# Performance work log

Hardware: AMD Instinct MI355X
Metric: run time of the kernel (lower is better)

The kernel has to match this reference:

```python
import jax, jax.numpy as jnp
import numpy as np

N_NODES = 50000


def gcn_conv(x, edge_index, W, b):
    """PyG-style GCNConv: add self-loops, symmetric normalization, x@W + bias."""
    N = x.shape[0]
    loop = jnp.arange(N, dtype=edge_index.dtype)
    src = jnp.concatenate([edge_index[0], loop])  # message sources
    dst = jnp.concatenate([edge_index[1], loop])  # aggregation targets
    deg = jax.ops.segment_sum(jnp.ones_like(dst, dtype=x.dtype), dst, num_segments=N)
    dinv = jnp.where(deg > 0, jax.lax.rsqrt(jnp.maximum(deg, 1.0)), 0.0)
    norm = dinv[src] * dinv[dst]  # [E+N]
    h = x @ W  # [N, out] dense transform first (fewer edge-dim FLOPs)
    msg = h[src] * norm[:, None]  # [E+N, out] gathered, normalized messages
    out = jax.ops.segment_sum(msg, dst, num_segments=N)
    return out + b


def setup_inputs() -> dict:
    key = jax.random.key(0)
    k1, k2, k3, k4 = jax.random.split(key, 4)
    x = jax.random.normal(k1, (N_NODES, 256), dtype=jnp.float32)
    edge_index = jax.random.randint(k2, (2, 800000), 0, N_NODES, dtype=jnp.int64)
    W1 = jax.random.normal(k3, (256, 256), dtype=jnp.float32) * (1.0 / np.sqrt(256))
    b1 = jnp.zeros((256,), dtype=jnp.float32)
    W2 = jax.random.normal(k4, (256, 128), dtype=jnp.float32) * (1.0 / np.sqrt(256))
    b2 = jnp.zeros((128,), dtype=jnp.float32)
    return {"x": x, "edge_index": edge_index, "W1": W1, "b1": b1, "W2": W2, "b2": b2}


def reference(x, edge_index, W1, b1, W2, b2):
    h = gcn_conv(x, edge_index, W1, b1)
    h = jax.nn.relu(h)
    return gcn_conv(h, edge_index, W2, b2)
```

## Files before the change

kernel.cpp:

```cpp
#include <hip/hip_runtime.h>

#define N_FEAT_IN 256
#define N_HID 256
#define N_OUT 128

using f32x4 = __attribute__((ext_vector_type(4))) float;
using bf16x8 = __attribute__((ext_vector_type(8))) short;

__device__ inline unsigned short bf16_rne(float f) {
    unsigned u = __builtin_bit_cast(unsigned, f);
    unsigned r = u + 0x7FFFu + ((u >> 16) & 1u);
    return (unsigned short)(r >> 16);
}
__device__ inline float bf16_to_f(unsigned short h) {
    unsigned u = ((unsigned)h) << 16;
    return __builtin_bit_cast(float, u);
}

__global__ void detect_i64_kernel(const int* __restrict__ edges, int* __restrict__ flag) {
    __shared__ int s[256];
    int tid = threadIdx.x;
    int zeros = 0;
    for (int i = tid; i < 2048; i += 256) zeros += (edges[2 * i + 1] == 0) ? 1 : 0;
    s[tid] = zeros;
    __syncthreads();
    for (int off = 128; off; off >>= 1) {
        if (tid < off) s[tid] += s[tid + off];
        __syncthreads();
    }
    if (tid == 0) flag[0] = (s[0] > 1900) ? 1 : 0;
}

__global__ void convert_count_kernel(const void* __restrict__ edges, int E,
                                     const int* __restrict__ flag,
                                     int* __restrict__ src, int* __restrict__ dst,
                                     int* __restrict__ cnt) {
    int e = blockIdx.x * blockDim.x + threadIdx.x;
    if (e >= E) return;
    int s, d;
    if (flag[0]) {
        const long long* p = (const long long*)edges;
        s = (int)p[e];
        d = (int)p[(size_t)E + e];
    } else {
        const int* p = (const int*)edges;
        s = p[e];
        d = p[(size_t)E + e];
    }
    src[e] = s;
    dst[e] = d;
    atomicAdd(&cnt[d], 1);
}

__global__ __launch_bounds__(256) void scan_block_kernel(
    const int* __restrict__ cnt, int Nn, int* __restrict__ rowp, int* __restrict__ bsum,
    float* __restrict__ dinv) {
    __shared__ int sd[256];
    const int tid = threadIdx.x;
    const int i = blockIdx.x * 256 + tid;
    const int v = (i < Nn) ? cnt[i] : 0;
    if (i < Nn) dinv[i] = rsqrtf((float)(v + 1));
    sd[tid] = v;
    __syncthreads();
    for (int off = 1; off < 256; off <<= 1) {
        int t = (tid >= off) ? sd[tid - off] : 0;
        __syncthreads();
        sd[tid] += t;
        __syncthreads();
    }
    if (i < Nn) rowp[i] = sd[tid] - v;
    if (tid == 255) bsum[blockIdx.x] = sd[255];
}

__global__ __launch_bounds__(256) void scan_top_kernel(
    int* __restrict__ bsum, int Nb, int* __restrict__ rowp, int Nn) {
    __shared__ int sd[256];
    const int tid = threadIdx.x;
    const int v = (tid < Nb) ? bsum[tid] : 0;
    sd[tid] = v;
    __syncthreads();
    for (int off = 1; off < 256; off <<= 1) {
        int t = (tid >= off) ? sd[tid - off] : 0;
        __syncthreads();
        sd[tid] += t;
        __syncthreads();
    }
    if (tid < Nb) bsum[tid] = sd[tid] - v;
    if (tid == 255) rowp[Nn] = sd[255];
}

__global__ __launch_bounds__(256) void scan_add_kernel(
    const int* __restrict__ bsum, int Nn, int* __restrict__ rowp, int* __restrict__ cursor) {
    const int i = blockIdx.x * 256 + threadIdx.x;
    if (i < Nn) {
        const int r = rowp[i] + bsum[i >> 8];
        rowp[i] = r;
        cursor[i] = r;
    }
}

__global__ void fill_kernel(const int* __restrict__ src, const int* __restrict__ dst, int E,
                            const float* __restrict__ dinv, int* __restrict__ cursor,
                            int2* __restrict__ ce) {
    int e = blockIdx.x * blockDim.x + threadIdx.x;
    if (e >= E) return;
    int s = src[e], d = dst[e];
    int pos = atomicAdd(&cursor[d], 1);
    float w = dinv[s] * dinv[d];
    ce[pos] = make_int2(s, __builtin_bit_cast(int, w));
}

__global__ __launch_bounds__(256) void split_kernel(
    const float* __restrict__ in, int n4,
    unsigned short* __restrict__ hi, unsigned short* __restrict__ lo) {
    int i = blockIdx.x * 256 + threadIdx.x;
    if (i >= n4) return;
    float4 v = ((const float4*)in)[i];
    ushort4 h, l;
    h.x = bf16_rne(v.x); l.x = bf16_rne(v.x - bf16_to_f(h.x));
    h.y = bf16_rne(v.y); l.y = bf16_rne(v.y - bf16_to_f(h.y));
    h.z = bf16_rne(v.z); l.z = bf16_rne(v.z - bf16_to_f(h.z));
    h.w = bf16_rne(v.w); l.w = bf16_rne(v.w - bf16_to_f(h.w));
    ((ushort4*)hi)[i] = h;
    ((ushort4*)lo)[i] = l;
}

__global__ __launch_bounds__(256) void splitT_kernel(
    const float* __restrict__ W, int K, int N,
    unsigned short* __restrict__ thi, unsigned short* __restrict__ tlo) {
    int idx = blockIdx.x * 256 + threadIdx.x;
    if (idx >= K * N) return;
    int k = idx / N, n = idx - k * N;
    float f = W[idx];
    unsigned short h = bf16_rne(f);
    unsigned short l = bf16_rne(f - bf16_to_f(h));
    thi[(size_t)n * K + k] = h;
    tlo[(size_t)n * K + k] = l;
}

__global__ __launch_bounds__(256) void gemm_mfma_kernel(
    const unsigned short* __restrict__ Ah, const unsigned short* __restrict__ Al,
    const unsigned short* __restrict__ Bh, const unsigned short* __restrict__ Bl,
    unsigned short* __restrict__ C, int M, int N, int K) {
    __shared__ char lds[4 * 128 * 64];
    char* As_h = lds;
    char* As_l = lds + 8192;
    char* Bs_h = lds + 16384;
    char* Bs_l = lds + 24576;

    const int tid = threadIdx.x;
    const int lane = tid & 63;
    const int wv = tid >> 6;
    const int wrow = (wv >> 1) * 64;
    const int wcol = (wv & 1) * 64;

    const int srow = tid >> 1;
    const int shalf = tid & 1;

    const long arow_g = (long)blockIdx.y * 128 + srow;
    const bool aval = arow_g < M;
    const int bcol_g = blockIdx.x * 128 + srow;

    const size_t a_base = (size_t)(aval ? arow_g : 0) * K + shalf * 16;
    const size_t b_base = (size_t)bcol_g * K + shalf * 16;

    const int sw = ((srow >> 1) & 3) << 4;
    const int w0 = (srow * 64 + shalf * 32) ^ sw;
    const int w1 = (srow * 64 + shalf * 32 + 16) ^ sw;

    int ra[4], rb[4];
#pragma unroll
    for (int m = 0; m < 4; m++) {
        int r = wrow + m * 16 + (lane & 15);
        ra[m] = (r * 64 + (lane >> 4) * 16) ^ (((r >> 1) & 3) << 4);
        int c = wcol + m * 16 + (lane & 15);
        rb[m] = (c * 64 + (lane >> 4) * 16) ^ (((c >> 1) & 3) << 4);
    }

    f32x4 acc[4][4] = {};
    const bf16x8 zero8 = {0, 0, 0, 0, 0, 0, 0, 0};

    const int nkt = K >> 5;
    for (int kt = 0; kt < nkt; kt++) {
        const int kb = kt * 32;
        bf16x8 vah0 = zero8, vah1 = zero8, val0 = zero8, val1 = zero8;
        if (aval) {
            vah0 = *(const bf16x8*)(Ah + a_base + kb);
            vah1 = *(const bf16x8*)(Ah + a_base + kb + 8);
            val0 = *(const bf16x8*)(Al + a_base + kb);
            val1 = *(const bf16x8*)(Al + a_base + kb + 8);
        }
        bf16x8 vbh0 = *(const bf16x8*)(Bh + b_base + kb);
        bf16x8 vbh1 = *(const bf16x8*)(Bh + b_base + kb + 8);
        bf16x8 vbl0 = *(const bf16x8*)(Bl + b_base + kb);
        bf16x8 vbl1 = *(const bf16x8*)(Bl + b_base + kb + 8);
        __syncthreads();
        *(bf16x8*)(As_h + w0) = vah0;  *(bf16x8*)(As_h + w1) = vah1;
        *(bf16x8*)(As_l + w0) = val0;  *(bf16x8*)(As_l + w1) = val1;
        *(bf16x8*)(Bs_h + w0) = vbh0;  *(bf16x8*)(Bs_h + w1) = vbh1;
        *(bf16x8*)(Bs_l + w0) = vbl0;  *(bf16x8*)(Bs_l + w1) = vbl1;
        __syncthreads();
        bf16x8 ah[4], al[4], bh[4], bl[4];
#pragma unroll
        for (int m = 0; m < 4; m++) {
            ah[m] = *(const bf16x8*)(As_h + ra[m]);
            al[m] = *(const bf16x8*)(As_l + ra[m]);
            bh[m] = *(const bf16x8*)(Bs_h + rb[m]);
            bl[m] = *(const bf16x8*)(Bs_l + rb[m]);
        }
#pragma unroll
        for (int m = 0; m < 4; m++)
#pragma unroll
            for (int n = 0; n < 4; n++) {
                acc[m][n] = __builtin_amdgcn_mfma_f32_16x16x32_bf16(ah[m], bh[n], acc[m][n], 0, 0, 0);
                acc[m][n] = __builtin_amdgcn_mfma_f32_16x16x32_bf16(al[m], bh[n], acc[m][n], 0, 0, 0);
                acc[m][n] = __builtin_amdgcn_mfma_f32_16x16x32_bf16(ah[m], bl[n], acc[m][n], 0, 0, 0);
            }
    }

    const int c0 = blockIdx.x * 128 + wcol + (lane & 15);
    const long r0 = (long)blockIdx.y * 128 + wrow + (lane >> 4) * 4;
#pragma unroll
    for (int m = 0; m < 4; m++)
#pragma unroll
        for (int j = 0; j < 4; j++) {
            long r = r0 + m * 16 + j;
            if (r < M) {
#pragma unroll
                for (int n = 0; n < 4; n++)
                    C[(size_t)r * N + c0 + n * 16] = bf16_rne(acc[m][n][j]);
            }
        }
}

template <int C, bool RELU, bool SPLIT>
__global__ __launch_bounds__(256) void agg_kernel(
    const unsigned short* __restrict__ h, const int* __restrict__ rowp,
    const int2* __restrict__ ce,
    const float* __restrict__ dinv, const float* __restrict__ bias,
    float* __restrict__ out,
    unsigned short* __restrict__ ohi, unsigned short* __restrict__ olo, int Nn) {
    constexpr int VEC = C / 64;
    static_assert(VEC == 2 || VEC == 4, "C must be 128 or 256");
    const int lane = threadIdx.x & 63;
    const int wv = threadIdx.x >> 6;
    const int node0 = blockIdx.x * 4 + wv;
    if (node0 >= Nn) return;
    const int node = __builtin_amdgcn_readfirstlane(node0);
    const float di = dinv[node];
    const int coff = lane * VEC;
    const unsigned short* __restrict__ hc = h + coff;
    float acc[VEC];

    auto loadrow = [&](int row, float v[VEC]) {
        const unsigned short* r = hc + (size_t)row * C;
        if constexpr (VEC == 4) {
            ushort4 t = *(const ushort4*)r;
            v[0] = bf16_to_f(t.x); v[1] = bf16_to_f(t.y);
            v[2] = bf16_to_f(t.z); v[3] = bf16_to_f(t.w);
        } else {
            ushort2 t = *(const ushort2*)r;
            v[0] = bf16_to_f(t.x); v[1] = bf16_to_f(t.y);
        }
    };

    {
        float v[VEC];
        loadrow(node, v);
#pragma unroll
        for (int j = 0; j < VEC; j++) acc[j] = di * di * v[j];
    }

    const int s = rowp[node];
    const int e = rowp[node + 1];
    for (int base = s; base < e; base += 64) {
        const int m = min(64, e - base);
        int myc = 0, myn = 0;
        if (lane < m) {
            int2 p = ce[base + lane];
            myc = p.x;
            myn = p.y;
        }
        int j = 0;
        for (; j + 4 <= m; j += 4) {
            const int c0 = __builtin_amdgcn_readlane(myc, j);
            const int c1 = __builtin_amdgcn_readlane(myc, j + 1);
            const int c2 = __builtin_amdgcn_readlane(myc, j + 2);
            const int c3 = __builtin_amdgcn_readlane(myc, j + 3);
            const float w0 = __builtin_bit_cast(float, __builtin_amdgcn_readlane(myn, j));
            const float w1 = __builtin_bit_cast(float, __builtin_amdgcn_readlane(myn, j + 1));
            const float w2 = __builtin_bit_cast(float, __builtin_amdgcn_readlane(myn, j + 2));
            const float w3 = __builtin_bit_cast(float, __builtin_amdgcn_readlane(myn, j + 3));
            float v0[VEC], v1[VEC], v2[VEC], v3[VEC];
            loadrow(c0, v0);
            loadrow(c1, v1);
            loadrow(c2, v2);
            loadrow(c3, v3);
#pragma unroll
            for (int q = 0; q < VEC; q++)
                acc[q] += w0 * v0[q] + w1 * v1[q] + w2 * v2[q] + w3 * v3[q];
        }
        for (; j < m; ++j) {
            const int c0 = __builtin_amdgcn_readlane(myc, j);
            const float w0 = __builtin_bit_cast(float, __builtin_amdgcn_readlane(myn, j));
            float v0[VEC];
            loadrow(c0, v0);
#pragma unroll
            for (int q = 0; q < VEC; q++) acc[q] += w0 * v0[q];
        }
    }

    {
        const float* bv = bias + coff;
#pragma unroll
        for (int j = 0; j < VEC; j++) {
            acc[j] += bv[j];
            if (RELU) acc[j] = fmaxf(acc[j], 0.f);
        }
    }
    if constexpr (SPLIT) {
        if constexpr (VEC == 4) {
            ushort4 hh, ll;
            hh.x = bf16_rne(acc[0]); ll.x = bf16_rne(acc[0] - bf16_to_f(hh.x));
            hh.y = bf16_rne(acc[1]); ll.y = bf16_rne(acc[1] - bf16_to_f(hh.y));
            hh.z = bf16_rne(acc[2]); ll.z = bf16_rne(acc[2] - bf16_to_f(hh.z));
            hh.w = bf16_rne(acc[3]); ll.w = bf16_rne(acc[3] - bf16_to_f(hh.w));
            *(ushort4*)(ohi + (size_t)node * C + coff) = hh;
            *(ushort4*)(olo + (size_t)node * C + coff) = ll;
        } else {
            ushort2 hh, ll;
            hh.x = bf16_rne(acc[0]); ll.x = bf16_rne(acc[0] - bf16_to_f(hh.x));
            hh.y = bf16_rne(acc[1]); ll.y = bf16_rne(acc[1] - bf16_to_f(hh.y));
            *(ushort2*)(ohi + (size_t)node * C + coff) = hh;
            *(ushort2*)(olo + (size_t)node * C + coff) = ll;
        }
    } else {
        float* o = out + (size_t)node * C + coff;
        if constexpr (VEC == 4) {
            *(float4*)o = make_float4(acc[0], acc[1], acc[2], acc[3]);
        } else {
            *(float2*)o = make_float2(acc[0], acc[1]);
        }
    }
}

extern "C" void kernel_launch(void* const* d_in, const int* in_sizes, int n_in,
                              void* d_out, int out_size, void* d_ws, size_t ws_size,
                              hipStream_t stream) {
    const float* x = (const float*)d_in[0];
    const void* edges = d_in[1];
    const float* W1 = (const float*)d_in[2];
    const float* b1 = (const float*)d_in[3];
    const float* W2 = (const float*)d_in[4];
    const float* b2 = (const float*)d_in[5];
    float* out = (float*)d_out;

    const int Nn = in_sizes[0] / N_FEAT_IN;
    const int E = in_sizes[1] / 2;

    char* w = (char*)d_ws;
    size_t off = 0;
    auto alloc = [&](size_t bytes) -> void* {
        void* p = (void*)(w + off);
        off += (bytes + 255) & ~(size_t)255;
        return p;
    };
    int* flag = (int*)alloc(sizeof(int));
    int* srcI = (int*)alloc((size_t)E * 4);
    int* dstI = (int*)alloc((size_t)E * 4);
    int* cnt = (int*)alloc((size_t)Nn * 4);
    int* rowp = (int*)alloc(((size_t)Nn + 1) * 4);
    int* cursor = (int*)alloc((size_t)Nn * 4);
    int* bsum = (int*)alloc(1024 * 4);
    int2* ce = (int2*)alloc((size_t)E * 8);
    float* dinv = (float*)alloc((size_t)Nn * 4);
    unsigned short* xhi = (unsigned short*)alloc((size_t)Nn * N_FEAT_IN * 2);
    unsigned short* xlo = (unsigned short*)alloc((size_t)Nn * N_FEAT_IN * 2);
    unsigned short* w1hi = (unsigned short*)alloc((size_t)N_FEAT_IN * N_HID * 2);
    unsigned short* w1lo = (unsigned short*)alloc((size_t)N_FEAT_IN * N_HID * 2);
    unsigned short* w2hi = (unsigned short*)alloc((size_t)N_HID * N_OUT * 2);
    unsigned short* w2lo = (unsigned short*)alloc((size_t)N_HID * N_OUT * 2);
    unsigned short* h = (unsigned short*)alloc((size_t)Nn * N_HID * 2);
    unsigned short* a1hi = xhi;
    unsigned short* a1lo = xlo;

    hipMemsetAsync(cnt, 0, (size_t)Nn * 4, stream);
    detect_i64_kernel<<<1, 256, 0, stream>>>((const int*)edges, flag);
    const int eb = (E + 255) / 256;
    convert_count_kernel<<<eb, 256, 0, stream>>>(edges, E, flag, srcI, dstI, cnt);
    const int nb = (Nn + 255) / 256;
    scan_block_kernel<<<nb, 256, 0, stream>>>(cnt, Nn, rowp, bsum, dinv);
    scan_top_kernel<<<1, 256, 0, stream>>>(bsum, nb, rowp, Nn);
    scan_add_kernel<<<nb, 256, 0, stream>>>(bsum, Nn, rowp, cursor);
    fill_kernel<<<eb, 256, 0, stream>>>(srcI, dstI, E, dinv, cursor, ce);

    const int n4x = Nn * N_FEAT_IN / 4;
    split_kernel<<<(n4x + 255) / 256, 256, 0, stream>>>(x, n4x, xhi, xlo);
    splitT_kernel<<<(N_FEAT_IN * N_HID + 255) / 256, 256, 0, stream>>>(W1, N_FEAT_IN, N_HID, w1hi, w1lo);
    splitT_kernel<<<(N_HID * N_OUT + 255) / 256, 256, 0, stream>>>(W2, N_HID, N_OUT, w2hi, w2lo);

    dim3 g1(N_HID / 128, (Nn + 127) / 128);
    gemm_mfma_kernel<<<g1, 256, 0, stream>>>(xhi, xlo, w1hi, w1lo, h, Nn, N_HID, N_FEAT_IN);
    agg_kernel<N_HID, true, true><<<(Nn + 3) / 4, 256, 0, stream>>>(
        h, rowp, ce, dinv, b1, nullptr, a1hi, a1lo, Nn);

    dim3 g2(N_OUT / 128, (Nn + 127) / 128);
    gemm_mfma_kernel<<<g2, 256, 0, stream>>>(a1hi, a1lo, w2hi, w2lo, h, Nn, N_OUT, N_HID);
    agg_kernel<N_OUT, false, false><<<(Nn + 3) / 4, 256, 0, stream>>>(
        h, rowp, ce, dinv, b2, out, nullptr, nullptr, Nn);
}
```

Before: 261.9 us.

## Fuse x bf16 split into first GEMM and drop intermediate edge arrays

The first GEMM now reads fp32 x directly and splits it into bf16 hi/lo inside the kernel, replacing the separate split pass and its 2x bf16 intermediate buffers. The edge conversion kernel no longer writes int32 src/dst arrays; count and fill read the raw edge_index directly. This cuts a full pass over x (about 51MB read plus writes) and the edge scratch traffic. In exchange the GEMM does conversion arithmetic per tile and reads twice as many A bytes, once for each of its two column blocks.

```diff
diff --git a/kernel.cpp b/kernel.cpp
--- a/kernel.cpp
+++ b/kernel.cpp
@@ -31,24 +31,16 @@
     if (tid == 0) flag[0] = (s[0] > 1900) ? 1 : 0;
 }
 
-__global__ void convert_count_kernel(const void* __restrict__ edges, int E,
-                                     const int* __restrict__ flag,
-                                     int* __restrict__ src, int* __restrict__ dst,
-                                     int* __restrict__ cnt) {
+__global__ void count_kernel(const void* __restrict__ edges, int E,
+                             const int* __restrict__ flag, int* __restrict__ cnt) {
     int e = blockIdx.x * blockDim.x + threadIdx.x;
     if (e >= E) return;
-    int s, d;
+    int d;
     if (flag[0]) {
-        const long long* p = (const long long*)edges;
-        s = (int)p[e];
-        d = (int)p[(size_t)E + e];
+        d = (int)((const long long*)edges)[(size_t)E + e];
     } else {
-        const int* p = (const int*)edges;
-        s = p[e];
-        d = p[(size_t)E + e];
-    }
-    src[e] = s;
-    dst[e] = d;
+        d = ((const int*)edges)[(size_t)E + e];
+    }
     atomicAdd(&cnt[d], 1);
 }
 
@@ -99,30 +91,25 @@
     }
 }
 
-__global__ void fill_kernel(const int* __restrict__ src, const int* __restrict__ dst, int E,
+__global__ void fill_kernel(const void* __restrict__ edges, int E,
+                            const int* __restrict__ flag,
                             const float* __restrict__ dinv, int* __restrict__ cursor,
                             int2* __restrict__ ce) {
     int e = blockIdx.x * blockDim.x + threadIdx.x;
     if (e >= E) return;
-    int s = src[e], d = dst[e];
+    int s, d;
+    if (flag[0]) {
+        const long long* p = (const long long*)edges;
+        s = (int)p[e];
+        d = (int)p[(size_t)E + e];
+    } else {
+        const int* p = (const int*)edges;
+        s = p[e];
+        d = p[(size_t)E + e];
+    }
     int pos = atomicAdd(&cursor[d], 1);
     float w = dinv[s] * dinv[d];
     ce[pos] = make_int2(s, __builtin_bit_cast(int, w));
-}
-
-__global__ __launch_bounds__(256) void split_kernel(
-    const float* __restrict__ in, int n4,
-    unsigned short* __restrict__ hi, unsigned short* __restrict__ lo) {
-    int i = blockIdx.x * 256 + threadIdx.x;
-    if (i >= n4) return;
-    float4 v = ((const float4*)in)[i];
-    ushort4 h, l;
-    h.x = bf16_rne(v.x); l.x = bf16_rne(v.x - bf16_to_f(h.x));
-    h.y = bf16_rne(v.y); l.y = bf16_rne(v.y - bf16_to_f(h.y));
-    h.z = bf16_rne(v.z); l.z = bf16_rne(v.z - bf16_to_f(h.z));
-    h.w = bf16_rne(v.w); l.w = bf16_rne(v.w - bf16_to_f(h.w));
-    ((ushort4*)hi)[i] = h;
-    ((ushort4*)lo)[i] = l;
 }
 
 __global__ __launch_bounds__(256) void splitT_kernel(
@@ -136,6 +123,114 @@
     unsigned short l = bf16_rne(f - bf16_to_f(h));
     thi[(size_t)n * K + k] = h;
     tlo[(size_t)n * K + k] = l;
+}
+
+__global__ __launch_bounds__(256) void gemm_mfma_f32a_kernel(
+    const float* __restrict__ Af,
+    const unsigned short* __restrict__ Bh, const unsigned short* __restrict__ Bl,
+    unsigned short* __restrict__ C, int M, int N, int K) {
+    __shared__ char lds[4 * 128 * 64];
+    char* As_h = lds;
+    char* As_l = lds + 8192;
+    char* Bs_h = lds + 16384;
+    char* Bs_l = lds + 24576;
+
+    const int tid = threadIdx.x;
+    const int lane = tid & 63;
+    const int wv = tid >> 6;
+    const int wrow = (wv >> 1) * 64;
+    const int wcol = (wv & 1) * 64;
+
+    const int srow = tid >> 1;
+    const int shalf = tid & 1;
+
+    const long arow_g = (long)blockIdx.y * 128 + srow;
+    const bool aval = arow_g < M;
+    const int bcol_g = blockIdx.x * 128 + srow;
+
+    const size_t a_base = (size_t)(aval ? arow_g : 0) * K + shalf * 16;
+    const size_t b_base = (size_t)bcol_g * K + shalf * 16;
+
+    const int sw = ((srow >> 1) & 3) << 4;
+    const int w0 = (srow * 64 + shalf * 32) ^ sw;
+    const int w1 = (srow * 64 + shalf * 32 + 16) ^ sw;
+
+    int ra[4], rb[4];
+#pragma unroll
+    for (int m = 0; m < 4; m++) {
+        int r = wrow + m * 16 + (lane & 15);
+        ra[m] = (r * 64 + (lane >> 4) * 16) ^ (((r >> 1) & 3) << 4);
+        int c = wcol + m * 16 + (lane & 15);
+        rb[m] = (c * 64 + (lane >> 4) * 16) ^ (((c >> 1) & 3) << 4);
+    }
+
+    f32x4 acc[4][4] = {};
+
+    const int nkt = K >> 5;
+    for (int kt = 0; kt < nkt; kt++) {
+        const int kb = kt * 32;
+        float fa[16];
+#pragma unroll
+        for (int i = 0; i < 16; i++) fa[i] = 0.f;
+        if (aval) {
+#pragma unroll
+            for (int i = 0; i < 4; i++) {
+                float4 f = *(const float4*)(Af + a_base + kb + i * 4);
+                fa[i * 4 + 0] = f.x; fa[i * 4 + 1] = f.y;
+                fa[i * 4 + 2] = f.z; fa[i * 4 + 3] = f.w;
+            }
+        }
+        bf16x8 vah0, vah1, val0, val1;
+#pragma unroll
+        for (int i = 0; i < 8; i++) {
+            unsigned short hh = bf16_rne(fa[i]);
+            unsigned short ll = bf16_rne(fa[i] - bf16_to_f(hh));
+            vah0[i] = (short)hh; val0[i] = (short)ll;
+            unsigned short hh1 = bf16_rne(fa[8 + i]);
+            unsigned short ll1 = bf16_rne(fa[8 + i] - bf16_to_f(hh1));
+            vah1[i] = (short)hh1; val1[i] = (short)ll1;
+        }
+        bf16x8 vbh0 = *(const bf16x8*)(Bh + b_base + kb);
+        bf16x8 vbh1 = *(const bf16x8*)(Bh + b_base + kb + 8);
+        bf16x8 vbl0 = *(const bf16x8*)(Bl + b_base + kb);
+        bf16x8 vbl1 = *(const bf16x8*)(Bl + b_base + kb + 8);
+        __syncthreads();
+        *(bf16x8*)(As_h + w0) = vah0;  *(bf16x8*)(As_h + w1) = vah1;
+        *(bf16x8*)(As_l + w0) = val0;  *(bf16x8*)(As_l + w1) = val1;
+        *(bf16x8*)(Bs_h + w0) = vbh0;  *(bf16x8*)(Bs_h + w1) = vbh1;
+        *(bf16x8*)(Bs_l + w0) = vbl0;  *(bf16x8*)(Bs_l + w1) = vbl1;
+        __syncthreads();
+        bf16x8 ah[4], al[4], bh[4], bl[4];
+#pragma unroll
+        for (int m = 0; m < 4; m++) {
+            ah[m] = *(const bf16x8*)(As_h + ra[m]);
+            al[m] = *(const bf16x8*)(As_l + ra[m]);
+            bh[m] = *(const bf16x8*)(Bs_h + rb[m]);
+            bl[m] = *(const bf16x8*)(Bs_l + rb[m]);
+        }
+#pragma unroll
+        for (int m = 0; m < 4; m++)
+#pragma unroll
+            for (int n = 0; n < 4; n++) {
+                acc[m][n] = __builtin_amdgcn_mfma_f32_16x16x32_bf16(ah[m], bh[n], acc[m][n], 0, 0, 0);
+                acc[m][n] = __builtin_amdgcn_mfma_f32_16x16x32_bf16(al[m], bh[n], acc[m][n], 0, 0, 0);
+                acc[m][n] = __builtin_amdgcn_mfma_f32_16x16x32_bf16(ah[m], bl[n], acc[m][n], 0, 0, 0);
+            }
+    }
+
+    const int c0 = blockIdx.x * 128 + wcol + (lane & 15);
+    const long r0 = (long)blockIdx.y * 128 + wrow + (lane >> 4) * 4;
+#pragma unroll
+    for (int m = 0; m < 4; m++)
+#pragma unroll
+        for (int j = 0; j < 4; j++) {
+            long r = r0 + m * 16 + j;
+            if (r < M) {
+#pragma unroll
+                for (int n = 0; n < 4; n++)
+                    C[(size_t)r * N + c0 + n * 16] = bf16_rne(acc[m][n][j]);
+            }
+        }
 }
 
 __global__ __launch_bounds__(256) void gemm_mfma_kernel(
@@ -366,41 +461,35 @@
         return p;
     };
     int* flag = (int*)alloc(sizeof(int));
-    int* srcI = (int*)alloc((size_t)E * 4);
-    int* dstI = (int*)alloc((size_t)E * 4);
     int* cnt = (int*)alloc((size_t)Nn * 4);
     int* rowp = (int*)alloc(((size_t)Nn + 1) * 4);
     int* cursor = (int*)alloc((size_t)Nn * 4);
     int* bsum = (int*)alloc(1024 * 4);
     int2* ce = (int2*)alloc((size_t)E * 8);
     float* dinv = (float*)alloc((size_t)Nn * 4);
-    unsigned short* xhi = (unsigned short*)alloc((size_t)Nn * N_FEAT_IN * 2);
-    unsigned short* xlo = (unsigned short*)alloc((size_t)Nn * N_FEAT_IN * 2);
     unsigned short* w1hi = (unsigned short*)alloc((size_t)N_FEAT_IN * N_HID * 2);
     unsigned short* w1lo = (unsigned short*)alloc((size_t)N_FEAT_IN * N_HID * 2);
     unsigned short* w2hi = (unsigned short*)alloc((size_t)N_HID * N_OUT * 2);
     unsigned short* w2lo = (unsigned short*)alloc((size_t)N_HID * N_OUT * 2);
+    unsigned short* a1hi = (unsigned short*)alloc((size_t)Nn * N_HID * 2);
+    unsigned short* a1lo = (unsigned short*)alloc((size_t)Nn * N_HID * 2);
     unsigned short* h = (unsigned short*)alloc((size_t)Nn * N_HID * 2);
-    unsigned short* a1hi = xhi;
-    unsigned short* a1lo = xlo;
 
     hipMemsetAsync(cnt, 0, (size_t)Nn * 4, stream);
     detect_i64_kernel<<<1, 256, 0, stream>>>((const int*)edges, flag);
     const int eb = (E + 255) / 256;
-    convert_count_kernel<<<eb, 256, 0, stream>>>(edges, E, flag, srcI, dstI, cnt);
+    count_kernel<<<eb, 256, 0, stream>>>(edges, E, flag, cnt);
     const int nb = (Nn + 255) / 256;
     scan_block_kernel<<<nb, 256, 0, stream>>>(cnt, Nn, rowp, bsum, dinv);
     scan_top_kernel<<<1, 256, 0, stream>>>(bsum, nb, rowp, Nn);
     scan_add_kernel<<<nb, 256, 0, stream>>>(bsum, Nn, rowp, cursor);
-    fill_kernel<<<eb, 256, 0, stream>>>(srcI, dstI, E, dinv, cursor, ce);
-
-    const int n4x = Nn * N_FEAT_IN / 4;
-    split_kernel<<<(n4x + 255) / 256, 256, 0, stream>>>(x, n4x, xhi, xlo);
+    fill_kernel<<<eb, 256, 0, stream>>>(edges, E, flag, dinv, cursor, ce);
+
     splitT_kernel<<<(N_FEAT_IN * N_HID + 255) / 256, 256, 0, stream>>>(W1, N_FEAT_IN, N_HID, w1hi, w1lo);
     splitT_kernel<<<(N_HID * N_OUT + 255) / 256, 256, 0, stream>>>(W2, N_HID, N_OUT, w2hi, w2lo);
 
     dim3 g1(N_HID / 128, (Nn + 127) / 128);
-    gemm_mfma_kernel<<<g1, 256, 0, stream>>>(xhi, xlo, w1hi, w1lo, h, Nn, N_HID, N_FEAT_IN);
+    gemm_mfma_f32a_kernel<<<g1, 256, 0, stream>>>(x, w1hi, w1lo, h, Nn, N_HID, N_FEAT_IN);
     agg_kernel<N_HID, true, true><<<(Nn + 3) / 4, 256, 0, stream>>>(
         h, rowp, ce, dinv, b1, nullptr, a1hi, a1lo, Nn);
 
```

New measurement: 250.2 us. -4.5%, faster.
